# Performance work log

Measured on AMD Instinct MI355X. Metric: run time of the kernel, lower is better.

## Reference

```python
import jax, jax.numpy as jnp
import numpy as np

N_NODES = 100000

def setup_inputs() -> dict:
    key = jax.random.key(0)
    k1, k2, k3, k4 = jax.random.split(key, 4)
    B, S, D, H = 50000, 10, 128, 128
    nodes = jax.random.randint(k1, (B,), 0, N_NODES, dtype=jnp.int64 if jax.config.jax_enable_x64 else jnp.int32)
    neigh_idx = jax.random.randint(k2, (B, S), 0, N_NODES, dtype=nodes.dtype)
    feature = jax.random.normal(k3, (N_NODES, D), dtype=jnp.float32)
    weight = jax.random.normal(k4, (2 * D, H), dtype=jnp.float32) * (1.0 / np.sqrt(2 * D))
    return {"nodes": nodes, "neigh_idx": neigh_idx, "feature": feature, "weight": weight}

def reference(nodes, neigh_idx, feature, weight):
    # Mean aggregation over sampled neighbors: [B, S, D] -> [B, D]
    neigh_feats = jnp.mean(feature[neigh_idx], axis=1)
    # Self features: [B, D]
    self_feats = feature[nodes]
    # Concat + linear + ReLU (gcn=False branch)
    combined = jnp.concatenate([self_feats, neigh_feats], axis=1)  # [B, 2D]
    return jax.nn.relu(combined @ weight)  # [B, H]
```

## Files before the change

### kernel.cpp

```cpp
#include <hip/hip_runtime.h>


typedef __attribute__((ext_vector_type(8))) short bf16x8;
typedef __attribute__((ext_vector_type(4))) float f32x4;

__device__ __forceinline__ unsigned short f2bf(float x) {
  unsigned int u = __float_as_uint(x);
  u += 0x7fffu + ((u >> 16) & 1u);
  return (unsigned short)(u >> 16);
}

__global__ void sage_prep_wt(const float* __restrict__ W,
                             unsigned short* __restrict__ Wt) {
  int tid = blockIdx.x * blockDim.x + threadIdx.x;
  float4 v = ((const float4*)W)[tid];
  int flat = tid << 2;
  int k = flat >> 7;
  int h = flat & 127;
  Wt[(h + 0) * 256 + k] = f2bf(v.x);
  Wt[(h + 1) * 256 + k] = f2bf(v.y);
  Wt[(h + 2) * 256 + k] = f2bf(v.z);
  Wt[(h + 3) * 256 + k] = f2bf(v.w);
}

__global__ __launch_bounds__(512, 6)
void sage_fused3(const int* __restrict__ nodes,
                 const int* __restrict__ neigh,
                 const float* __restrict__ feat,
                 const unsigned short* __restrict__ Wt,
                 float* __restrict__ out, int B)
{
  constexpr int K = 256, H = 128, S = 10;
  constexpr int TILE = 32;
  constexpr int STR = K + 8;
  __shared__ unsigned short Clds[TILE * STR];

  const int t = threadIdx.x;
  const int block0 = blockIdx.x * TILE;

  {
    const int r   = t >> 4;
    const int sub = t & 15;
    const int b   = block0 + r;
    unsigned short* crow = &Clds[r * STR];
    if (b < B) {
      const float4* f4 = (const float4*)feat;
      const long srow = (long)nodes[b] * 32;
      float4 s0 = f4[srow + sub];
      float4 s1 = f4[srow + 16 + sub];

      float ax0=0.f, ay0=0.f, az0=0.f, aw0=0.f;
      float ax1=0.f, ay1=0.f, az1=0.f, aw1=0.f;
#pragma unroll
      for (int s = 0; s < S; ++s) {
        const long nrow = (long)neigh[b * S + s] * 32;
        float4 v0 = f4[nrow + sub];
        float4 v1 = f4[nrow + 16 + sub];
        ax0 += v0.x; ay0 += v0.y; az0 += v0.z; aw0 += v0.w;
        ax1 += v1.x; ay1 += v1.y; az1 += v1.z; aw1 += v1.w;
      }
      ushort4 o;
      o.x = f2bf(s0.x); o.y = f2bf(s0.y); o.z = f2bf(s0.z); o.w = f2bf(s0.w);
      *(ushort4*)&crow[4 * sub] = o;
      o.x = f2bf(s1.x); o.y = f2bf(s1.y); o.z = f2bf(s1.z); o.w = f2bf(s1.w);
      *(ushort4*)&crow[64 + 4 * sub] = o;
      o.x = f2bf(ax0 * 0.1f); o.y = f2bf(ay0 * 0.1f);
      o.z = f2bf(az0 * 0.1f); o.w = f2bf(aw0 * 0.1f);
      *(ushort4*)&crow[128 + 4 * sub] = o;
      o.x = f2bf(ax1 * 0.1f); o.y = f2bf(ay1 * 0.1f);
      o.z = f2bf(az1 * 0.1f); o.w = f2bf(aw1 * 0.1f);
      *(ushort4*)&crow[192 + 4 * sub] = o;
    } else {
      ushort4 z; z.x = z.y = z.z = z.w = 0;
      *(ushort4*)&crow[4 * sub] = z;
      *(ushort4*)&crow[64 + 4 * sub] = z;
      *(ushort4*)&crow[128 + 4 * sub] = z;
      *(ushort4*)&crow[192 + 4 * sub] = z;
    }
  }
  __syncthreads();
  __builtin_amdgcn_sched_barrier(0);

  const int lane = t & 63;
  const int wave = t >> 6;
  const int m    = lane & 15;
  const int quad = lane >> 4;
  const int cbase = wave * 16;

  bf16x8 bfrag[8];
#pragma unroll
  for (int ks = 0; ks < 8; ++ks)
    bfrag[ks] = *(const bf16x8*)&Wt[(cbase + m) * K + ks * 32 + quad * 8];

  f32x4 acc0 = {0.f, 0.f, 0.f, 0.f};
  f32x4 acc1 = {0.f, 0.f, 0.f, 0.f};
#pragma unroll
  for (int ks = 0; ks < 8; ++ks) {
    const int koff = ks * 32 + quad * 8;
    bf16x8 a0 = *(const bf16x8*)&Clds[(m     ) * STR + koff];
    bf16x8 a1 = *(const bf16x8*)&Clds[(16 + m) * STR + koff];
    acc0 = __builtin_amdgcn_mfma_f32_16x16x32_bf16(a0, bfrag[ks], acc0, 0, 0, 0);
    acc1 = __builtin_amdgcn_mfma_f32_16x16x32_bf16(a1, bfrag[ks], acc1, 0, 0, 0);
  }

#pragma unroll
  for (int reg = 0; reg < 4; ++reg) {
    const int row0 = quad * 4 + reg;
    const int gb0 = block0 + row0;
    const int gb1 = gb0 + 16;
    if (gb0 < B) out[(size_t)gb0 * H + cbase + m] = fmaxf(acc0[reg], 0.0f);
    if (gb1 < B) out[(size_t)gb1 * H + cbase + m] = fmaxf(acc1[reg], 0.0f);
  }
}

extern "C" void kernel_launch(void* const* d_in, const int* in_sizes, int n_in,
                              void* d_out, int out_size, void* d_ws, size_t ws_size,
                              hipStream_t stream) {
  const int*   nodes = (const int*)d_in[0];
  const int*   neigh = (const int*)d_in[1];
  const float* feat  = (const float*)d_in[2];
  const float* W     = (const float*)d_in[3];
  float*       out   = (float*)d_out;
  const int B = in_sizes[0];

  unsigned short* Wt = (unsigned short*)d_ws;
  sage_prep_wt<<<32, 256, 0, stream>>>(W, Wt);
  const int grid = (B + 31) / 32;
  sage_fused3<<<grid, 512, 0, stream>>>(nodes, neigh, feat, Wt, out, B);
}
```

Baseline: 129.6 us.

## Halve rows per block and batch neighbor index and feature gathers

The block now processes 16 rows instead of 32, with 32 threads per row so each thread gathers one float4 per neighbor instead of two. All neighbor indices are loaded up front, and then all ten neighbor feature vectors are issued as independent loads before they are summed. This is meant to put more gather loads in flight and spread the work over twice as many blocks. In exchange, each block still reloads the full bf16 weight fragments, so weight traffic from L2 doubles, and each wave now runs only one MFMA tile instead of two.

```diff
diff --git a/kernel.cpp b/kernel.cpp
--- a/kernel.cpp
+++ b/kernel.cpp
@@ -24,14 +24,14 @@
 }
 
 __global__ __launch_bounds__(512, 6)
-void sage_fused3(const int* __restrict__ nodes,
+void sage_fused4(const int* __restrict__ nodes,
                  const int* __restrict__ neigh,
                  const float* __restrict__ feat,
                  const unsigned short* __restrict__ Wt,
                  float* __restrict__ out, int B)
 {
   constexpr int K = 256, H = 128, S = 10;
-  constexpr int TILE = 32;
+  constexpr int TILE = 16;
   constexpr int STR = K + 8;
   __shared__ unsigned short Clds[TILE * STR];
 
@@ -39,43 +39,37 @@
   const int block0 = blockIdx.x * TILE;
 
   {
-    const int r   = t >> 4;
-    const int sub = t & 15;
+    const int r   = t >> 5;
+    const int sub = t & 31;
     const int b   = block0 + r;
     unsigned short* crow = &Clds[r * STR];
     if (b < B) {
       const float4* f4 = (const float4*)feat;
+
+      int nidx[S];
+#pragma unroll
+      for (int s = 0; s < S; ++s) nidx[s] = neigh[b * S + s];
       const long srow = (long)nodes[b] * 32;
-      float4 s0 = f4[srow + sub];
-      float4 s1 = f4[srow + 16 + sub];
 
-      float ax0=0.f, ay0=0.f, az0=0.f, aw0=0.f;
-      float ax1=0.f, ay1=0.f, az1=0.f, aw1=0.f;
+      float4 self = f4[srow + sub];
+      float4 v[S];
 #pragma unroll
-      for (int s = 0; s < S; ++s) {
-        const long nrow = (long)neigh[b * S + s] * 32;
-        float4 v0 = f4[nrow + sub];
-        float4 v1 = f4[nrow + 16 + sub];
-        ax0 += v0.x; ay0 += v0.y; az0 += v0.z; aw0 += v0.w;
-        ax1 += v1.x; ay1 += v1.y; az1 += v1.z; aw1 += v1.w;
-      }
+      for (int s = 0; s < S; ++s) v[s] = f4[(long)nidx[s] * 32 + sub];
+
+      float ax = 0.f, ay = 0.f, az = 0.f, aw = 0.f;
+#pragma unroll
+      for (int s = 0; s < S; ++s) { ax += v[s].x; ay += v[s].y; az += v[s].z; aw += v[s].w; }
+
       ushort4 o;
-      o.x = f2bf(s0.x); o.y = f2bf(s0.y); o.z = f2bf(s0.z); o.w = f2bf(s0.w);
+      o.x = f2bf(self.x); o.y = f2bf(self.y); o.z = f2bf(self.z); o.w = f2bf(self.w);
       *(ushort4*)&crow[4 * sub] = o;
-      o.x = f2bf(s1.x); o.y = f2bf(s1.y); o.z = f2bf(s1.z); o.w = f2bf(s1.w);
-      *(ushort4*)&crow[64 + 4 * sub] = o;
-      o.x = f2bf(ax0 * 0.1f); o.y = f2bf(ay0 * 0.1f);
-      o.z = f2bf(az0 * 0.1f); o.w = f2bf(aw0 * 0.1f);
+      o.x = f2bf(ax * 0.1f); o.y = f2bf(ay * 0.1f);
+      o.z = f2bf(az * 0.1f); o.w = f2bf(aw * 0.1f);
       *(ushort4*)&crow[128 + 4 * sub] = o;
-      o.x = f2bf(ax1 * 0.1f); o.y = f2bf(ay1 * 0.1f);
-      o.z = f2bf(az1 * 0.1f); o.w = f2bf(aw1 * 0.1f);
-      *(ushort4*)&crow[192 + 4 * sub] = o;
     } else {
       ushort4 z; z.x = z.y = z.z = z.w = 0;
       *(ushort4*)&crow[4 * sub] = z;
-      *(ushort4*)&crow[64 + 4 * sub] = z;
       *(ushort4*)&crow[128 + 4 * sub] = z;
-      *(ushort4*)&crow[192 + 4 * sub] = z;
     }
   }
   __syncthreads();
@@ -92,24 +86,17 @@
   for (int ks = 0; ks < 8; ++ks)
     bfrag[ks] = *(const bf16x8*)&Wt[(cbase + m) * K + ks * 32 + quad * 8];
 
-  f32x4 acc0 = {0.f, 0.f, 0.f, 0.f};
-  f32x4 acc1 = {0.f, 0.f, 0.f, 0.f};
+  f32x4 acc = {0.f, 0.f, 0.f, 0.f};
 #pragma unroll
   for (int ks = 0; ks < 8; ++ks) {
-    const int koff = ks * 32 + quad * 8;
-    bf16x8 a0 = *(const bf16x8*)&Clds[(m     ) * STR + koff];
-    bf16x8 a1 = *(const bf16x8*)&Clds[(16 + m) * STR + koff];
-    acc0 = __builtin_amdgcn_mfma_f32_16x16x32_bf16(a0, bfrag[ks], acc0, 0, 0, 0);
-    acc1 = __builtin_amdgcn_mfma_f32_16x16x32_bf16(a1, bfrag[ks], acc1, 0, 0, 0);
+    bf16x8 a = *(const bf16x8*)&Clds[m * STR + ks * 32 + quad * 8];
+    acc = __builtin_amdgcn_mfma_f32_16x16x32_bf16(a, bfrag[ks], acc, 0, 0, 0);
   }
 
 #pragma unroll
   for (int reg = 0; reg < 4; ++reg) {
-    const int row0 = quad * 4 + reg;
-    const int gb0 = block0 + row0;
-    const int gb1 = gb0 + 16;
-    if (gb0 < B) out[(size_t)gb0 * H + cbase + m] = fmaxf(acc0[reg], 0.0f);
-    if (gb1 < B) out[(size_t)gb1 * H + cbase + m] = fmaxf(acc1[reg], 0.0f);
+    const int gb = block0 + quad * 4 + reg;
+    if (gb < B) out[(size_t)gb * H + cbase + m] = fmaxf(acc[reg], 0.0f);
   }
 }
 
@@ -125,6 +112,6 @@
 
   unsigned short* Wt = (unsigned short*)d_ws;
   sage_prep_wt<<<32, 256, 0, stream>>>(W, Wt);
-  const int grid = (B + 31) / 32;
-  sage_fused3<<<grid, 512, 0, stream>>>(nodes, neigh, feat, Wt, out, B);
+  const int grid = (B + 15) / 16;
+  sage_fused4<<<grid, 512, 0, stream>>>(nodes, neigh, feat, Wt, out, B);
 }
```

Result: slower. 139.2 us (+7.4%).
